# Optimization experiments

Hardware: AMD Instinct MI355X
Metric: run time of the kernel (lower is better)

## Reference

```python
import jax, jax.numpy as jnp
import numpy as np

EMBED_DIM = 1024
NUM_HEADS = 16
DEPTH = EMBED_DIM // NUM_HEADS


def setup_inputs() -> dict:
    key = jax.random.key(0)
    ks = jax.random.split(key, 6)
    B, S, D = 2, 2048, EMBED_DIM
    scale = 1.0 / np.sqrt(D)
    return {
        "x": jax.random.normal(ks[0], (B, S, D), dtype=jnp.float32),
        "mask": jax.random.randint(ks[1], (B, S), 0, 2, dtype=jnp.int32),
        "wq_w": jax.random.normal(ks[2], (D, D), dtype=jnp.float32) * scale,
        "wq_b": jnp.zeros((D,), dtype=jnp.float32),
        "wk_w": jax.random.normal(ks[3], (D, D), dtype=jnp.float32) * scale,
        "wk_b": jnp.zeros((D,), dtype=jnp.float32),
        "wv_w": jax.random.normal(ks[4], (D, D), dtype=jnp.float32) * scale,
        "wv_b": jnp.zeros((D,), dtype=jnp.float32),
        "dense_w": jax.random.normal(ks[5], (D, D), dtype=jnp.float32) * scale,
        "dense_b": jnp.zeros((D,), dtype=jnp.float32),
    }


def _split_heads(t, B, S):
    # [B, S, D] -> [B, H, S, depth]
    return t.reshape(B, S, NUM_HEADS, DEPTH).transpose(0, 2, 1, 3)


def reference(x, mask, wq_w, wq_b, wk_w, wk_b, wv_w, wv_b, dense_w, dense_b):
    B, S, D = x.shape
    q = _split_heads(x @ wq_w.T + wq_b, B, S)  # [B, H, S, d]
    k = _split_heads(x @ wk_w.T + wk_b, B, S)
    v = _split_heads(x @ wv_w.T + wv_b, B, S)

    logits = jnp.einsum('bhqd,bhkd->bhqk', q, k) / jnp.sqrt(
        jnp.asarray(DEPTH, dtype=jnp.float32))
    # mask [B, S] broadcast to [B, 1, 1, S] over key axis, additive -1e9
    logits = logits + mask.astype(logits.dtype)[:, None, None, :] * (-1e9)
    attn = jax.nn.softmax(logits, axis=-1)  # [B, H, S, S]
    ctx = jnp.einsum('bhqk,bhkd->bhqd', attn, v)
    ctx = ctx.transpose(0, 2, 1, 3).reshape(B, S, D)
    out = ctx @ dense_w.T + dense_b
    return out, attn
```

## Files before the change

### kernel.cpp

```cpp
#include <hip/hip_runtime.h>


#define S_LEN 2048
#define D_DIM 1024
#define H_NUM 16
#define M_ROWS 4096

typedef __attribute__((ext_vector_type(8))) short bf16x8;
typedef __attribute__((ext_vector_type(4))) float f32x4;

static __device__ __forceinline__ unsigned short f2bf(float f) {
  union { float f; unsigned u; } v; v.f = f;
  unsigned r = (v.u + 0x7FFFu + ((v.u >> 16) & 1u)) >> 16;
  return (unsigned short)r;
}

static __device__ __forceinline__ bf16x8 cvt8(float4 a, float4 b) {
  bf16x8 r;
  r[0] = (short)f2bf(a.x); r[1] = (short)f2bf(a.y);
  r[2] = (short)f2bf(a.z); r[3] = (short)f2bf(a.w);
  r[4] = (short)f2bf(b.x); r[5] = (short)f2bf(b.y);
  r[6] = (short)f2bf(b.z); r[7] = (short)f2bf(b.w);
  return r;
}

static __device__ __forceinline__ void gld16(const void* g, void* s) {
  __builtin_amdgcn_global_load_lds(
      (const __attribute__((address_space(1))) unsigned int*)g,
      (__attribute__((address_space(3))) unsigned int*)s, 16, 0, 0);
}

__global__ __launch_bounds__(256) void cast_f32_bf16(
    const float* __restrict__ src, unsigned short* __restrict__ dst, int n4) {
  int i = blockIdx.x * 256 + threadIdx.x;
  if (i >= n4) return;
  float4 v = ((const float4*)src)[i];
  unsigned long long o =
      (unsigned long long)f2bf(v.x) |
      ((unsigned long long)f2bf(v.y) << 16) |
      ((unsigned long long)f2bf(v.z) << 32) |
      ((unsigned long long)f2bf(v.w) << 48);
  ((unsigned long long*)dst)[i] = o;
}

__global__ __launch_bounds__(256) void gemm_qkv(
    const unsigned short* __restrict__ A,
    const unsigned short* __restrict__ W0, const unsigned short* __restrict__ W1,
    const unsigned short* __restrict__ W2,
    const float* __restrict__ b0, const float* __restrict__ b1,
    const float* __restrict__ b2,
    unsigned short* __restrict__ C0, unsigned short* __restrict__ C1,
    unsigned short* __restrict__ C2) {
  const unsigned short* W = W0; const float* bias = b0; unsigned short* C = C0;
  if (blockIdx.z == 1) { W = W1; bias = b1; C = C1; }
  else if (blockIdx.z == 2) { W = W2; bias = b2; C = C2; }

  __shared__ __align__(16) unsigned short As[128 * 64];
  __shared__ __align__(16) unsigned short Bs[128 * 64];

  const int tid = threadIdx.x;
  const int l = tid & 63;
  const int w = tid >> 6;
  const int wm = w >> 1, wn = w & 1;
  const int lo = l & 15, hi = l >> 4;

  const int mBase = blockIdx.y * 128;
  const int nBase = blockIdx.x * 128;

  f32x4 acc[4][4];
  for (int mr = 0; mr < 4; ++mr)
    for (int nr = 0; nr < 4; ++nr) acc[mr][nr] = (f32x4){0.f, 0.f, 0.f, 0.f};

  for (int k0 = 0; k0 < 1024; k0 += 64) {
    __syncthreads();
    for (int i = 0; i < 4; ++i) {
      int s = w * 4 + i;
      int row = s * 8 + (l >> 3), colb = (l & 7) * 8;
      gld16(A + (size_t)(mBase + row) * 1024 + k0 + colb, As + s * 512);
      gld16(W + (size_t)(nBase + row) * 1024 + k0 + colb, Bs + s * 512);
    }
    __syncthreads();
    for (int kk = 0; kk < 2; ++kk) {
      bf16x8 af[4], bfm[4];
      for (int mr = 0; mr < 4; ++mr)
        af[mr] = *(const bf16x8*)&As[(wm * 64 + mr * 16 + lo) * 64 + kk * 32 + hi * 8];
      for (int nr = 0; nr < 4; ++nr)
        bfm[nr] = *(const bf16x8*)&Bs[(wn * 64 + nr * 16 + lo) * 64 + kk * 32 + hi * 8];
      for (int mr = 0; mr < 4; ++mr)
        for (int nr = 0; nr < 4; ++nr)
          acc[mr][nr] = __builtin_amdgcn_mfma_f32_16x16x32_bf16(
              af[mr], bfm[nr], acc[mr][nr], 0, 0, 0);
    }
  }

  if (blockIdx.z == 2) {
    for (int nr = 0; nr < 4; ++nr) {
      int col = nBase + wn * 64 + nr * 16 + lo;
      float bv = bias[col];
      int hh = col >> 6, dd = col & 63;
      for (int mr = 0; mr < 4; ++mr) {
        int rbase = mBase + wm * 64 + mr * 16 + hi * 4;
        int bb = rbase >> 11, ss = rbase & 2047;
        unsigned long long o = 0;
        for (int i = 0; i < 4; ++i)
          o |= (unsigned long long)f2bf(acc[mr][nr][i] + bv) << (16 * i);
        *(unsigned long long*)(C +
            ((size_t)((bb * H_NUM + hh) * 64 + dd) * S_LEN + ss)) = o;
      }
    }
  } else {
    for (int nr = 0; nr < 4; ++nr) {
      int col = nBase + wn * 64 + nr * 16 + lo;
      float bv = bias[col];
      for (int mr = 0; mr < 4; ++mr) {
        int rbase = mBase + wm * 64 + mr * 16 + hi * 4;
        for (int i = 0; i < 4; ++i)
          C[(size_t)(rbase + i) * 1024 + col] = f2bf(acc[mr][nr][i] + bv);
      }
    }
  }
}

__global__ __launch_bounds__(256) void gemm_proj(
    const unsigned short* __restrict__ A, const float* __restrict__ W,
    const float* __restrict__ bias, float* __restrict__ C) {
  __shared__ __align__(16) unsigned short As[128][40];
  __shared__ __align__(16) unsigned short Bs[128][40];

  const int tid = threadIdx.x;
  const int l = tid & 63;
  const int w = tid >> 6;
  const int wm = w >> 1, wn = w & 1;
  const int lo = l & 15, hi = l >> 4;

  const int mBase = blockIdx.y * 128;
  const int nBase = blockIdx.x * 128;

  f32x4 acc[4][4];
  for (int mr = 0; mr < 4; ++mr)
    for (int nr = 0; nr < 4; ++nr) acc[mr][nr] = (f32x4){0.f, 0.f, 0.f, 0.f};

  for (int k0 = 0; k0 < 1024; k0 += 32) {
    __syncthreads();
    for (int it = 0; it < 2; ++it) {
      int c = tid + it * 256;
      int r = c >> 2, cc = (c & 3) * 8;
      *(int4*)&As[r][cc] = *(const int4*)(A + (size_t)(mBase + r) * 1024 + k0 + cc);
      const float* wp = W + (size_t)(nBase + r) * 1024 + k0 + cc;
      *(bf16x8*)&Bs[r][cc] = cvt8(((const float4*)wp)[0], ((const float4*)wp)[1]);
    }
    __syncthreads();
    bf16x8 af[4], bfm[4];
    for (int mr = 0; mr < 4; ++mr)
      af[mr] = *(const bf16x8*)&As[wm * 64 + mr * 16 + lo][hi * 8];
    for (int nr = 0; nr < 4; ++nr)
      bfm[nr] = *(const bf16x8*)&Bs[wn * 64 + nr * 16 + lo][hi * 8];
    for (int mr = 0; mr < 4; ++mr)
      for (int nr = 0; nr < 4; ++nr)
        acc[mr][nr] = __builtin_amdgcn_mfma_f32_16x16x32_bf16(
            af[mr], bfm[nr], acc[mr][nr], 0, 0, 0);
  }

  for (int nr = 0; nr < 4; ++nr) {
    int col = nBase + wn * 64 + nr * 16 + lo;
    float bv = bias[col];
    for (int mr = 0; mr < 4; ++mr) {
      int rbase = mBase + wm * 64 + mr * 16 + hi * 4;
      for (int i = 0; i < 4; ++i)
        C[(size_t)(rbase + i) * 1024 + col] = acc[mr][nr][i] + bv;
    }
  }
}

__global__ __launch_bounds__(256) void attn_kernel(
    const unsigned short* __restrict__ qb, const unsigned short* __restrict__ kb,
    const unsigned short* __restrict__ vT, const int* __restrict__ mask,
    float* __restrict__ attn, unsigned short* __restrict__ ctx) {
  const int bid = blockIdx.x;
  const int wid = (bid & 7) * 128 + (bid >> 3);
  const int q0 = (wid & 31) * 64;
  const int h  = (wid >> 5) & 15;
  const int b  = wid >> 9;

  const int tid = threadIdx.x, l = tid & 63, w = tid >> 6;
  const int lo = l & 15, hi = l >> 4;

  __shared__ __align__(16) unsigned short k_lds[64][72];
  __shared__ __align__(16) unsigned short vt_lds[64][72];
  __shared__ __align__(16) float p_f32[64][68];

  bf16x8 qa[2];
  {
    const size_t qrow = (size_t)(b * S_LEN + q0 + w * 16 + lo) * D_DIM + h * 64;
    qa[0] = *(const bf16x8*)(qb + qrow + hi * 8);
    qa[1] = *(const bf16x8*)(qb + qrow + 32 + hi * 8);
  }

  const size_t kvbase = (size_t)b * S_LEN * D_DIM + h * 64;
  const unsigned short* vTh = vT + (size_t)((b * H_NUM + h) * 64) * S_LEN;
  const int* maskb = mask + b * S_LEN;

  float rsum[4] = {0.f, 0.f, 0.f, 0.f};
  for (int kt = 0; kt < 32; ++kt) {
    const int key0 = kt * 64;
    __syncthreads();
#pragma unroll
    for (int it = 0; it < 2; ++it) {
      int c = tid + it * 256;
      int r = c >> 3, cc = (c & 7) * 8;
      *(int4*)&k_lds[r][cc] =
          *(const int4*)(kb + kvbase + (size_t)(key0 + r) * D_DIM + cc);
    }
    __syncthreads();
    f32x4 acc[4];
    for (int nr = 0; nr < 4; ++nr) acc[nr] = (f32x4){0.f, 0.f, 0.f, 0.f};
#pragma unroll
    for (int kk = 0; kk < 2; ++kk)
#pragma unroll
      for (int nr = 0; nr < 4; ++nr) {
        bf16x8 kf = *(const bf16x8*)&k_lds[nr * 16 + lo][kk * 32 + hi * 8];
        acc[nr] = __builtin_amdgcn_mfma_f32_16x16x32_bf16(qa[kk], kf, acc[nr], 0, 0, 0);
      }
    for (int nr = 0; nr < 4; ++nr) {
      float ma = maskb[key0 + nr * 16 + lo] ? -1e9f : 0.f;
      for (int i = 0; i < 4; ++i)
        rsum[i] += __expf(acc[nr][i] * 0.125f + ma);
    }
  }
  for (int m = 1; m < 16; m <<= 1)
    for (int i = 0; i < 4; ++i) rsum[i] += __shfl_xor(rsum[i], m);
  float inv[4];
  for (int i = 0; i < 4; ++i) inv[i] = 1.0f / rsum[i];

  f32x4 ctxacc[4];
  for (int dc = 0; dc < 4; ++dc) ctxacc[dc] = (f32x4){0.f, 0.f, 0.f, 0.f};
  const size_t attnbase = (size_t)(b * H_NUM + h) * S_LEN * S_LEN;

  for (int kt = 0; kt < 32; ++kt) {
    const int key0 = kt * 64;
    __syncthreads();
#pragma unroll
    for (int it = 0; it < 2; ++it) {
      int c = tid + it * 256;
      int r = c >> 3, cc = (c & 7) * 8;
      *(int4*)&k_lds[r][cc] =
          *(const int4*)(kb + kvbase + (size_t)(key0 + r) * D_DIM + cc);
      *(int4*)&vt_lds[r][cc] =
          *(const int4*)(vTh + (size_t)r * S_LEN + key0 + cc);
    }
    __syncthreads();
    f32x4 acc[4];
    for (int nr = 0; nr < 4; ++nr) acc[nr] = (f32x4){0.f, 0.f, 0.f, 0.f};
#pragma unroll
    for (int kk = 0; kk < 2; ++kk)
#pragma unroll
      for (int nr = 0; nr < 4; ++nr) {
        bf16x8 kf = *(const bf16x8*)&k_lds[nr * 16 + lo][kk * 32 + hi * 8];
        acc[nr] = __builtin_amdgcn_mfma_f32_16x16x32_bf16(qa[kk], kf, acc[nr], 0, 0, 0);
      }
    for (int nr = 0; nr < 4; ++nr) {
      float ma = maskb[key0 + nr * 16 + lo] ? -1e9f : 0.f;
      for (int i = 0; i < 4; ++i)
        p_f32[w * 16 + hi * 4 + i][nr * 16 + lo] =
            __expf(acc[nr][i] * 0.125f + ma) * inv[i];
    }
    __syncthreads();

    bf16x8 pa[2];
    for (int kk = 0; kk < 2; ++kk) {
      const float* pr = &p_f32[w * 16 + lo][kk * 32 + hi * 8];
      pa[kk] = cvt8(*(const float4*)pr, *(const float4*)(pr + 4));
    }
#pragma unroll
    for (int kk = 0; kk < 2; ++kk)
#pragma unroll
      for (int dc = 0; dc < 4; ++dc) {
        bf16x8 vf = *(const bf16x8*)&vt_lds[dc * 16 + lo][kk * 32 + hi * 8];
        ctxacc[dc] = __builtin_amdgcn_mfma_f32_16x16x32_bf16(
            pa[kk], vf, ctxacc[dc], 0, 0, 0);
      }

#pragma unroll
    for (int it = 0; it < 4; ++it) {
      int c = tid + it * 256;
      int r = c >> 4, cc = (c & 15) * 4;
      *(float4*)(attn + attnbase + (size_t)(q0 + r) * S_LEN + key0 + cc) =
          *(const float4*)&p_f32[r][cc];
    }
  }

  for (int dc = 0; dc < 4; ++dc) {
    int col = h * 64 + dc * 16 + lo;
    for (int i = 0; i < 4; ++i) {
      int row = q0 + w * 16 + hi * 4 + i;
      ctx[(size_t)(b * S_LEN + row) * D_DIM + col] = f2bf(ctxacc[dc][i]);
    }
  }
}

extern "C" void kernel_launch(void* const* d_in, const int* in_sizes, int n_in,
                              void* d_out, int out_size, void* d_ws, size_t ws_size,
                              hipStream_t stream) {
  const float* x    = (const float*)d_in[0];
  const int*   mask = (const int*)d_in[1];
  const float* wq   = (const float*)d_in[2];
  const float* bq   = (const float*)d_in[3];
  const float* wk   = (const float*)d_in[4];
  const float* bk   = (const float*)d_in[5];
  const float* wv   = (const float*)d_in[6];
  const float* bv   = (const float*)d_in[7];
  const float* wd   = (const float*)d_in[8];
  const float* bd   = (const float*)d_in[9];

  float* out  = (float*)d_out;
  float* attn = out + (size_t)M_ROWS * D_DIM;

  unsigned short* xb  = (unsigned short*)attn;
  unsigned short* wqb = xb + 4194304;
  unsigned short* wkb = xb + 5242880;
  unsigned short* wvb = xb + 6291456;

  unsigned short* ws   = (unsigned short*)d_ws;
  unsigned short* qb   = ws;
  unsigned short* kbuf = ws + 4194304;
  unsigned short* vTb  = ws + 8388608;
  unsigned short* ctxb = ws + 12582912;

  cast_f32_bf16<<<4096, 256, 0, stream>>>(x,  xb,  1048576);
  cast_f32_bf16<<<1024, 256, 0, stream>>>(wq, wqb, 262144);
  cast_f32_bf16<<<1024, 256, 0, stream>>>(wk, wkb, 262144);
  cast_f32_bf16<<<1024, 256, 0, stream>>>(wv, wvb, 262144);

  gemm_qkv<<<dim3(8, 32, 3), 256, 0, stream>>>(
      xb, wqb, wkb, wvb, bq, bk, bv, qb, kbuf, vTb);

  attn_kernel<<<1024, 256, 0, stream>>>(qb, kbuf, vTb, mask, attn, ctxb);

  gemm_proj<<<dim3(8, 32), 256, 0, stream>>>(ctxb, wd, bd, out);
}
```

Baseline: 352.4 us.

## Fuse fp32-to-bf16 casts into QKV GEMM and shrink attention key tiles

Removes the four separate cast kernels and has the QKV GEMM load fp32 X and weights directly, converting to bf16 while staging into LDS, with a K-step of 32 and padded LDS rows. The attention kernel's second pass moves to 32-key tiles, stores probabilities as bf16 in LDS, drops one barrier, and writes the attn output by expanding those bf16 values back to fp32. It also drops the block-index swizzle. The attention output is now bf16-rounded, and the GEMM loses the async global_load_lds path and re-converts the weights for every tile.

```diff
diff --git a/kernel.cpp b/kernel.cpp
--- a/kernel.cpp
+++ b/kernel.cpp
@@ -24,39 +24,20 @@
   return r;
 }
 
-static __device__ __forceinline__ void gld16(const void* g, void* s) {
-  __builtin_amdgcn_global_load_lds(
-      (const __attribute__((address_space(1))) unsigned int*)g,
-      (__attribute__((address_space(3))) unsigned int*)s, 16, 0, 0);
-}
-
-__global__ __launch_bounds__(256) void cast_f32_bf16(
-    const float* __restrict__ src, unsigned short* __restrict__ dst, int n4) {
-  int i = blockIdx.x * 256 + threadIdx.x;
-  if (i >= n4) return;
-  float4 v = ((const float4*)src)[i];
-  unsigned long long o =
-      (unsigned long long)f2bf(v.x) |
-      ((unsigned long long)f2bf(v.y) << 16) |
-      ((unsigned long long)f2bf(v.z) << 32) |
-      ((unsigned long long)f2bf(v.w) << 48);
-  ((unsigned long long*)dst)[i] = o;
-}
-
-__global__ __launch_bounds__(256) void gemm_qkv(
-    const unsigned short* __restrict__ A,
-    const unsigned short* __restrict__ W0, const unsigned short* __restrict__ W1,
-    const unsigned short* __restrict__ W2,
+__global__ __launch_bounds__(256) void gemm_qkv3(
+    const float* __restrict__ X,
+    const float* __restrict__ W0, const float* __restrict__ W1,
+    const float* __restrict__ W2,
     const float* __restrict__ b0, const float* __restrict__ b1,
     const float* __restrict__ b2,
     unsigned short* __restrict__ C0, unsigned short* __restrict__ C1,
     unsigned short* __restrict__ C2) {
-  const unsigned short* W = W0; const float* bias = b0; unsigned short* C = C0;
+  const float* W = W0; const float* bias = b0; unsigned short* C = C0;
   if (blockIdx.z == 1) { W = W1; bias = b1; C = C1; }
   else if (blockIdx.z == 2) { W = W2; bias = b2; C = C2; }
 
-  __shared__ __align__(16) unsigned short As[128 * 64];
-  __shared__ __align__(16) unsigned short Bs[128 * 64];
+  __shared__ __align__(16) unsigned short As[128][40];
+  __shared__ __align__(16) unsigned short Bs[128][40];
 
   const int tid = threadIdx.x;
   const int l = tid & 63;
@@ -71,26 +52,26 @@
   for (int mr = 0; mr < 4; ++mr)
     for (int nr = 0; nr < 4; ++nr) acc[mr][nr] = (f32x4){0.f, 0.f, 0.f, 0.f};
 
-  for (int k0 = 0; k0 < 1024; k0 += 64) {
-    __syncthreads();
-    for (int i = 0; i < 4; ++i) {
-      int s = w * 4 + i;
-      int row = s * 8 + (l >> 3), colb = (l & 7) * 8;
-      gld16(A + (size_t)(mBase + row) * 1024 + k0 + colb, As + s * 512);
-      gld16(W + (size_t)(nBase + row) * 1024 + k0 + colb, Bs + s * 512);
-    }
-    __syncthreads();
-    for (int kk = 0; kk < 2; ++kk) {
-      bf16x8 af[4], bfm[4];
-      for (int mr = 0; mr < 4; ++mr)
-        af[mr] = *(const bf16x8*)&As[(wm * 64 + mr * 16 + lo) * 64 + kk * 32 + hi * 8];
+  for (int k0 = 0; k0 < 1024; k0 += 32) {
+    __syncthreads();
+    for (int it = 0; it < 2; ++it) {
+      int c = tid + it * 256;
+      int r = c >> 2, cc = (c & 3) * 8;
+      const float* ap = X + (size_t)(mBase + r) * 1024 + k0 + cc;
+      *(bf16x8*)&As[r][cc] = cvt8(((const float4*)ap)[0], ((const float4*)ap)[1]);
+      const float* wp = W + (size_t)(nBase + r) * 1024 + k0 + cc;
+      *(bf16x8*)&Bs[r][cc] = cvt8(((const float4*)wp)[0], ((const float4*)wp)[1]);
+    }
+    __syncthreads();
+    bf16x8 af[4], bfm[4];
+    for (int mr = 0; mr < 4; ++mr)
+      af[mr] = *(const bf16x8*)&As[wm * 64 + mr * 16 + lo][hi * 8];
+    for (int nr = 0; nr < 4; ++nr)
+      bfm[nr] = *(const bf16x8*)&Bs[wn * 64 + nr * 16 + lo][hi * 8];
+    for (int mr = 0; mr < 4; ++mr)
       for (int nr = 0; nr < 4; ++nr)
-        bfm[nr] = *(const bf16x8*)&Bs[(wn * 64 + nr * 16 + lo) * 64 + kk * 32 + hi * 8];
-      for (int mr = 0; mr < 4; ++mr)
-        for (int nr = 0; nr < 4; ++nr)
-          acc[mr][nr] = __builtin_amdgcn_mfma_f32_16x16x32_bf16(
-              af[mr], bfm[nr], acc[mr][nr], 0, 0, 0);
-    }
+        acc[mr][nr] = __builtin_amdgcn_mfma_f32_16x16x32_bf16(
+            af[mr], bfm[nr], acc[mr][nr], 0, 0, 0);
   }
 
   if (blockIdx.z == 2) {
@@ -177,17 +158,16 @@
     const unsigned short* __restrict__ vT, const int* __restrict__ mask,
     float* __restrict__ attn, unsigned short* __restrict__ ctx) {
   const int bid = blockIdx.x;
-  const int wid = (bid & 7) * 128 + (bid >> 3);
-  const int q0 = (wid & 31) * 64;
-  const int h  = (wid >> 5) & 15;
-  const int b  = wid >> 9;
+  const int q0 = (bid & 31) * 64;
+  const int h  = (bid >> 5) & 15;
+  const int b  = bid >> 9;
 
   const int tid = threadIdx.x, l = tid & 63, w = tid >> 6;
   const int lo = l & 15, hi = l >> 4;
 
   __shared__ __align__(16) unsigned short k_lds[64][72];
-  __shared__ __align__(16) unsigned short vt_lds[64][72];
-  __shared__ __align__(16) float p_f32[64][68];
+  __shared__ __align__(16) unsigned short vt_lds[64][40];
+  __shared__ __align__(16) unsigned short p_lds[64][40];
 
   bf16x8 qa[2];
   {
@@ -195,7 +175,6 @@
     qa[0] = *(const bf16x8*)(qb + qrow + hi * 8);
     qa[1] = *(const bf16x8*)(qb + qrow + 32 + hi * 8);
   }
-
   const size_t kvbase = (size_t)b * S_LEN * D_DIM + h * 64;
   const unsigned short* vTh = vT + (size_t)((b * H_NUM + h) * 64) * S_LEN;
   const int* maskb = mask + b * S_LEN;
@@ -236,56 +215,53 @@
   for (int dc = 0; dc < 4; ++dc) ctxacc[dc] = (f32x4){0.f, 0.f, 0.f, 0.f};
   const size_t attnbase = (size_t)(b * H_NUM + h) * S_LEN * S_LEN;
 
-  for (int kt = 0; kt < 32; ++kt) {
-    const int key0 = kt * 64;
-    __syncthreads();
-#pragma unroll
-    for (int it = 0; it < 2; ++it) {
-      int c = tid + it * 256;
-      int r = c >> 3, cc = (c & 7) * 8;
-      *(int4*)&k_lds[r][cc] =
-          *(const int4*)(kb + kvbase + (size_t)(key0 + r) * D_DIM + cc);
-      *(int4*)&vt_lds[r][cc] =
-          *(const int4*)(vTh + (size_t)r * S_LEN + key0 + cc);
-    }
-    __syncthreads();
-    f32x4 acc[4];
-    for (int nr = 0; nr < 4; ++nr) acc[nr] = (f32x4){0.f, 0.f, 0.f, 0.f};
+  for (int kt = 0; kt < 64; ++kt) {
+    const int key0 = kt * 32;
+    __syncthreads();
+    {
+      int rK = tid >> 3, cK = (tid & 7) * 8;
+      *(int4*)&k_lds[rK][cK] =
+          *(const int4*)(kb + kvbase + (size_t)(key0 + rK) * D_DIM + cK);
+      int rV = tid >> 2, cV = (tid & 3) * 8;
+      *(int4*)&vt_lds[rV][cV] =
+          *(const int4*)(vTh + (size_t)rV * S_LEN + key0 + cV);
+    }
+    __syncthreads();
+
+    f32x4 acc[2];
+    acc[0] = (f32x4){0.f, 0.f, 0.f, 0.f};
+    acc[1] = (f32x4){0.f, 0.f, 0.f, 0.f};
 #pragma unroll
     for (int kk = 0; kk < 2; ++kk)
 #pragma unroll
-      for (int nr = 0; nr < 4; ++nr) {
+      for (int nr = 0; nr < 2; ++nr) {
         bf16x8 kf = *(const bf16x8*)&k_lds[nr * 16 + lo][kk * 32 + hi * 8];
         acc[nr] = __builtin_amdgcn_mfma_f32_16x16x32_bf16(qa[kk], kf, acc[nr], 0, 0, 0);
       }
-    for (int nr = 0; nr < 4; ++nr) {
+#pragma unroll
+    for (int nr = 0; nr < 2; ++nr) {
       float ma = maskb[key0 + nr * 16 + lo] ? -1e9f : 0.f;
-      for (int i = 0; i < 4; ++i)
-        p_f32[w * 16 + hi * 4 + i][nr * 16 + lo] =
-            __expf(acc[nr][i] * 0.125f + ma) * inv[i];
-    }
-    __syncthreads();
-
-    bf16x8 pa[2];
-    for (int kk = 0; kk < 2; ++kk) {
-      const float* pr = &p_f32[w * 16 + lo][kk * 32 + hi * 8];
-      pa[kk] = cvt8(*(const float4*)pr, *(const float4*)(pr + 4));
-    }
-#pragma unroll
-    for (int kk = 0; kk < 2; ++kk)
-#pragma unroll
-      for (int dc = 0; dc < 4; ++dc) {
-        bf16x8 vf = *(const bf16x8*)&vt_lds[dc * 16 + lo][kk * 32 + hi * 8];
-        ctxacc[dc] = __builtin_amdgcn_mfma_f32_16x16x32_bf16(
-            pa[kk], vf, ctxacc[dc], 0, 0, 0);
-      }
-
-#pragma unroll
-    for (int it = 0; it < 4; ++it) {
-      int c = tid + it * 256;
-      int r = c >> 4, cc = (c & 15) * 4;
-      *(float4*)(attn + attnbase + (size_t)(q0 + r) * S_LEN + key0 + cc) =
-          *(const float4*)&p_f32[r][cc];
+      for (int i = 0; i < 4; ++i) {
+        float p = __expf(acc[nr][i] * 0.125f + ma) * inv[i];
+        p_lds[w * 16 + hi * 4 + i][nr * 16 + lo] = f2bf(p);
+      }
+    }
+    bf16x8 pa = *(const bf16x8*)&p_lds[w * 16 + lo][hi * 8];
+#pragma unroll
+    for (int dc = 0; dc < 4; ++dc) {
+      bf16x8 vf = *(const bf16x8*)&vt_lds[dc * 16 + lo][hi * 8];
+      ctxacc[dc] = __builtin_amdgcn_mfma_f32_16x16x32_bf16(pa, vf, ctxacc[dc], 0, 0, 0);
+    }
+#pragma unroll
+    for (int it = 0; it < 2; ++it) {
+      int row = w * 16 + it * 8 + (l >> 3);
+      int colb = (l & 7) * 4;
+      int2 pk = *(const int2*)&p_lds[row][colb];
+      union { unsigned u; float f; } e0, e1, e2, e3;
+      e0.u = (unsigned)pk.x << 16; e1.u = pk.x & 0xffff0000u;
+      e2.u = (unsigned)pk.y << 16; e3.u = pk.y & 0xffff0000u;
+      *(float4*)(attn + attnbase + (size_t)(q0 + row) * S_LEN + key0 + colb) =
+          (float4){e0.f, e1.f, e2.f, e3.f};
     }
   }
 
@@ -315,24 +291,14 @@
   float* out  = (float*)d_out;
   float* attn = out + (size_t)M_ROWS * D_DIM;
 
-  unsigned short* xb  = (unsigned short*)attn;
-  unsigned short* wqb = xb + 4194304;
-  unsigned short* wkb = xb + 5242880;
-  unsigned short* wvb = xb + 6291456;
-
   unsigned short* ws   = (unsigned short*)d_ws;
   unsigned short* qb   = ws;
   unsigned short* kbuf = ws + 4194304;
   unsigned short* vTb  = ws + 8388608;
   unsigned short* ctxb = ws + 12582912;
 
-  cast_f32_bf16<<<4096, 256, 0, stream>>>(x,  xb,  1048576);
-  cast_f32_bf16<<<1024, 256, 0, stream>>>(wq, wqb, 262144);
-  cast_f32_bf16<<<1024, 256, 0, stream>>>(wk, wkb, 262144);
-  cast_f32_bf16<<<1024, 256, 0, stream>>>(wv, wvb, 262144);
-
-  gemm_qkv<<<dim3(8, 32, 3), 256, 0, stream>>>(
-      xb, wqb, wkb, wvb, bq, bk, bv, qb, kbuf, vTb);
+  gemm_qkv3<<<dim3(8, 32, 3), 256, 0, stream>>>(
+      x, wq, wk, wv, bq, bk, bv, qb, kbuf, vTb);
 
   attn_kernel<<<1024, 256, 0, stream>>>(qb, kbuf, vTb, mask, attn, ctxb);
 
```

Measured after the change: 343.4 us. -2.6%, faster.
